# Kernel optimization log

Hardware: AMD Instinct MI355X
Metric: run time of the kernel (lower is better)

Reference implementation:

```python
import jax, jax.numpy as jnp
import numpy as np
import math

D_MODEL = 1024
N_DEVICES = 64
HIDDEN = 128
N_HEADS = 8
B, S = 16, 1024
W_SCALE = 0.02

def setup_inputs() -> dict:
    key = jax.random.key(0)
    ks = jax.random.split(key, 24)
    f = jax.random.normal
    inp = {
        'x': f(ks[0], (B, S, D_MODEL), jnp.float32),
        # attention pooling (n_heads=8, non-causal, self-attention) weights, stored [in,out]
        'wq': f(ks[1], (D_MODEL, D_MODEL), jnp.float32) * W_SCALE,
        'bq': jnp.zeros((D_MODEL,), jnp.float32),
        'wk': f(ks[2], (D_MODEL, D_MODEL), jnp.float32) * W_SCALE,
        'bk': jnp.zeros((D_MODEL,), jnp.float32),
        'wv': f(ks[3], (D_MODEL, D_MODEL), jnp.float32) * W_SCALE,
        'bv': jnp.zeros((D_MODEL,), jnp.float32),
        'wo': f(ks[4], (D_MODEL, D_MODEL), jnp.float32) * W_SCALE,
        'bo': jnp.zeros((D_MODEL,), jnp.float32),
        # device embedding table
        'emb': f(ks[5], (N_DEVICES, D_MODEL), jnp.float32),
        # routing gate: Linear(2d,d) -> Tanh -> Linear(d,N) -> Softmax
        'rg_w1': f(ks[6], (2 * D_MODEL, D_MODEL), jnp.float32) * W_SCALE,
        'rg_b1': jnp.zeros((D_MODEL,), jnp.float32),
        'rg_w2': f(ks[7], (D_MODEL, N_DEVICES), jnp.float32) * W_SCALE,
        'rg_b2': jnp.zeros((N_DEVICES,), jnp.float32),
        'reg_w1': f(ks[8], (N_DEVICES, D_MODEL, HIDDEN), jnp.float32) * W_SCALE,
        'reg_b1': jnp.zeros((N_DEVICES, HIDDEN), jnp.float32),
        'reg_w2': f(ks[9], (N_DEVICES, HIDDEN), jnp.float32) * W_SCALE,
        'reg_b2': jnp.zeros((N_DEVICES,), jnp.float32),
        # stacked per-device classification heads: Linear(d,h)->ReLU->Linear(h,1)->Sigmoid
        'cls_w1': f(ks[10], (N_DEVICES, D_MODEL, HIDDEN), jnp.float32) * W_SCALE,
        'cls_b1': jnp.zeros((N_DEVICES, HIDDEN), jnp.float32),
        'cls_w2': f(ks[11], (N_DEVICES, HIDDEN), jnp.float32) * W_SCALE,
        'cls_b2': jnp.zeros((N_DEVICES,), jnp.float32),
    }
    return inp


def _forward(x, wq, bq, wk, bk, wv, bv, wo, bo, emb,
             rg_w1, rg_b1, rg_w2, rg_b2,
             reg_w1, reg_b1, reg_w2, reg_b2,
             cls_w1, cls_b1, cls_w2, cls_b2):
    b, s, d = x.shape
    dk = d // N_HEADS
    scale = 1.0 / math.sqrt(dk)

    def split_heads(t):  # [b,s,d] -> [b,h,s,dk]
        return t.reshape(b, s, N_HEADS, dk).transpose(0, 2, 1, 3)

    Q = split_heads(x @ wq + bq)
    K = split_heads(x @ wk + bk)
    V = split_heads(x @ wv + bv)
    scores = jnp.einsum('bhqd,bhkd->bhqk', Q, K) * scale
    attn = jax.nn.softmax(scores, axis=-1)  # non-causal, no mask, eval (no dropout)
    ctx = jnp.einsum('bhqk,bhkd->bhqd', attn, V)
    ctx = ctx.transpose(0, 2, 1, 3).reshape(b, s, d)
    pooled = ctx @ wo + bo                       # [b,s,d]
    g = pooled.mean(axis=1)                      # [b,d] global_repr

    g_exp = jnp.broadcast_to(g[:, None, :], (b, N_DEVICES, d))
    de_exp = jnp.broadcast_to(emb[None, :, :], (b, N_DEVICES, d))

    # routing gate
    ri = jnp.concatenate([g_exp, de_exp], axis=-1)        # [b,N,2d]
    h = jnp.tanh(ri @ rg_w1 + rg_b1)                      # [b,N,d]
    rw = jax.nn.softmax(h @ rg_w2 + rg_b2, axis=-1)       # [b,N,N]
    device_repr = jnp.einsum('bnm,md->bnd', rw, emb)      # bmm with expanded embeds
    combined = g_exp + device_repr                        # [b,N,d]

    hr = jax.nn.relu(jnp.einsum('bnd,ndh->bnh', combined, reg_w1) + reg_b1)
    reg = jax.nn.softplus(jnp.einsum('bnh,nh->bn', hr, reg_w2) + reg_b2)

    # per-device classification heads (stacked)
    hc = jax.nn.relu(jnp.einsum('bnd,ndh->bnh', combined, cls_w1) + cls_b1)
    cls = jax.nn.sigmoid(jnp.einsum('bnh,nh->bn', hc, cls_w2) + cls_b2)
    return reg, cls


def reference(x, wq, bq, wk, bk, wv, bv, wo, bo, emb,
              rg_w1, rg_b1, rg_w2, rg_b2,
              reg_w1, reg_b1, reg_w2, reg_b2,
              cls_w1, cls_b1, cls_w2, cls_b2):
    return _forward(x, wq, bq, wk, bk, wv, bv, wo, bo, emb,
                    rg_w1, rg_b1, rg_w2, rg_b2,
                    reg_w1, reg_b1, reg_w2, reg_b2,
                    cls_w1, cls_b1, cls_w2, cls_b2)
```

## Files before the change

### kernel.cpp

```cpp
#include <hip/hip_runtime.h>

typedef unsigned short ushort_t;
typedef __attribute__((ext_vector_type(8))) short short8;
typedef __attribute__((ext_vector_type(4))) float floatx4;

__device__ __forceinline__ ushort_t f2bf(float f) {
    unsigned u = __float_as_uint(f);
    return (ushort_t)((u + 0x7fffu + ((u >> 16) & 1u)) >> 16);
}
__device__ __forceinline__ void gll16(const void* g, void* l) {
    __builtin_amdgcn_global_load_lds(
        (const __attribute__((address_space(1))) unsigned int*)g,
        (__attribute__((address_space(3))) unsigned int*)l, 16, 0, 0);
}

__global__ void prep_kernel(const float* __restrict__ x, ushort_t* __restrict__ xb) {
    size_t i = ((size_t)blockIdx.x * 256 + threadIdx.x) * 8;
    float4 v0 = *(const float4*)(x + i);
    float4 v1 = *(const float4*)(x + i + 4);
    uint4 o;
    o.x = (unsigned)f2bf(v0.x) | ((unsigned)f2bf(v0.y) << 16);
    o.y = (unsigned)f2bf(v0.z) | ((unsigned)f2bf(v0.w) << 16);
    o.z = (unsigned)f2bf(v1.x) | ((unsigned)f2bf(v1.y) << 16);
    o.w = (unsigned)f2bf(v1.z) | ((unsigned)f2bf(v1.w) << 16);
    *(uint4*)(xb + i) = o;
}

__global__ __launch_bounds__(256) void transpose_kernel(
    const float* __restrict__ wq, const float* __restrict__ wk,
    ushort_t* __restrict__ wqT, ushort_t* __restrict__ wkT)
{
    const float* src = blockIdx.z ? wk : wq;
    ushort_t* dst = blockIdx.z ? wkT : wqT;
    const int k0 = blockIdx.x * 64, n0 = blockIdx.y * 64;
    __shared__ float t[64][65];
    const int tid = threadIdx.x;
    const int rr = tid >> 4, cc = (tid & 15) * 4;
#pragma unroll
    for (int p = 0; p < 4; ++p) {
        float4 v = *(const float4*)(src + (size_t)(k0 + p * 16 + rr) * 1024 + n0 + cc);
        t[p * 16 + rr][cc + 0] = v.x;
        t[p * 16 + rr][cc + 1] = v.y;
        t[p * 16 + rr][cc + 2] = v.z;
        t[p * 16 + rr][cc + 3] = v.w;
    }
    __syncthreads();
#pragma unroll
    for (int p = 0; p < 4; ++p) {
        int nl = p * 16 + rr;
        uint2 o;
        o.x = (unsigned)f2bf(t[cc + 0][nl]) | ((unsigned)f2bf(t[cc + 1][nl]) << 16);
        o.y = (unsigned)f2bf(t[cc + 2][nl]) | ((unsigned)f2bf(t[cc + 3][nl]) << 16);
        *(uint2*)(dst + (size_t)(n0 + nl) * 1024 + k0 + cc) = o;
    }
}

__global__ __launch_bounds__(256) void gemm_qk_kernel(
    const ushort_t* __restrict__ xb, const ushort_t* __restrict__ wqT, const ushort_t* __restrict__ wkT,
    const float* __restrict__ bq, const float* __restrict__ bk,
    ushort_t* __restrict__ Qb, ushort_t* __restrict__ Kb)
{
    const int bm = blockIdx.x;
    const int bn = blockIdx.y;
    const int mat = blockIdx.z;
    const ushort_t* W = mat ? wkT : wqT;
    const float* bias = mat ? bk : bq;
    ushort_t* Out = mat ? Kb : Qb;
    const float postscale = mat ? 1.0f : 0.08838834764831845f;

    __shared__ ushort_t a_lds[2][128 * 32];
    __shared__ ushort_t b_lds[2][128 * 32];

    const int tid = threadIdx.x;
    const int lane = tid & 63;
    const int wave = tid >> 6;
    const int wr = wave >> 1, wc = wave & 1;
    const int l16 = lane & 15, quad = lane >> 4;

    floatx4 acc[4][4];
    const floatx4 zero4 = {0.f, 0.f, 0.f, 0.f};
#pragma unroll
    for (int i = 0; i < 4; ++i)
#pragma unroll
        for (int j = 0; j < 4; ++j) acc[i][j] = zero4;

    const int srow = wave * 32 + (lane >> 2);
    const int skof = (lane & 3) * 8;
    const ushort_t* gA = xb + (size_t)(bm * 128 + srow) * 1024 + skof;
    const ushort_t* gB = W + (size_t)(bn * 128 + srow) * 1024 + skof;

    auto issue = [&](int buf, int k0) {
        ushort_t* lA = &a_lds[buf][wave * 1024];
        ushort_t* lB = &b_lds[buf][wave * 1024];
        gll16(gA + k0, lA);
        gll16(gA + k0 + 16 * 1024, lA + 512);
        gll16(gB + k0, lB);
        gll16(gB + k0 + 16 * 1024, lB + 512);
    };

    issue(0, 0);
    for (int kt = 0; kt < 32; ++kt) {
        __syncthreads();
        if (kt < 31) issue((kt + 1) & 1, (kt + 1) * 32);
        const ushort_t* la = a_lds[kt & 1];
        const ushort_t* lb = b_lds[kt & 1];
        short8 afr[4], bfr[4];
#pragma unroll
        for (int mi = 0; mi < 4; ++mi)
            afr[mi] = *(const short8*)&la[(wr * 64 + mi * 16 + l16) * 32 + quad * 8];
#pragma unroll
        for (int ni = 0; ni < 4; ++ni)
            bfr[ni] = *(const short8*)&lb[(wc * 64 + ni * 16 + l16) * 32 + quad * 8];
#pragma unroll
        for (int mi = 0; mi < 4; ++mi)
#pragma unroll
            for (int ni = 0; ni < 4; ++ni)
                acc[mi][ni] = __builtin_amdgcn_mfma_f32_16x16x32_bf16(afr[mi], bfr[ni], acc[mi][ni], 0, 0, 0);
    }
#pragma unroll
    for (int mi = 0; mi < 4; ++mi) {
#pragma unroll
        for (int ni = 0; ni < 4; ++ni) {
            const int gcol = bn * 128 + wc * 64 + ni * 16 + l16;
            const int h = gcol >> 7, d = gcol & 127;
#pragma unroll
            for (int r = 0; r < 4; ++r) {
                const int grow = bm * 128 + wr * 64 + mi * 16 + quad * 4 + r;
                const int b = grow >> 10, s = grow & 1023;
                Out[(((size_t)(b * 8 + h)) * 1024 + s) * 128 + d] =
                    f2bf((acc[mi][ni][r] + bias[gcol]) * postscale);
            }
        }
    }
}

__global__ __launch_bounds__(256, 4) void attn_mfma_kernel(
    const ushort_t* __restrict__ Qb,
    const ushort_t* __restrict__ Kb,
    float* __restrict__ wout)
{
    const int bh = blockIdx.x;
    const int qt = blockIdx.y;
    __shared__ ushort_t ks[2][64 * 128];

    const int tid = threadIdx.x;
    const int wave = tid >> 6, lane = tid & 63;
    const int l16 = lane & 15, quad = lane >> 4;

    const ushort_t* Ksrc = Kb + (size_t)bh * 1024 * 128;

    int srcoff[4];
#pragma unroll
    for (int c = 0; c < 4; ++c) {
        int r = wave * 16 + c * 4 + (lane >> 4);
        int g = (lane & 15) ^ (r & 15);
        srcoff[c] = r * 128 + g * 8;
    }

    auto issue = [&](int buf, int kt) {
        const ushort_t* src = Ksrc + (size_t)kt * 8192;
#pragma unroll
        for (int c = 0; c < 4; ++c)
            gll16(src + srcoff[c], &ks[buf][(wave * 4 + c) * 512]);
    };

    short8 aq[2][4];
    {
        const ushort_t* qsrc = Qb + ((size_t)bh * 1024 + qt * 128 + wave * 32) * 128;
#pragma unroll
        for (int mi = 0; mi < 2; ++mi)
#pragma unroll
            for (int ksp = 0; ksp < 4; ++ksp)
                aq[mi][ksp] = *(const short8*)(qsrc + (size_t)(mi * 16 + l16) * 128 + ksp * 32 + quad * 8);
    }

    const floatx4 zero4 = {0.f, 0.f, 0.f, 0.f};
    float lsum[2][4];
#pragma unroll
    for (int mi = 0; mi < 2; ++mi)
#pragma unroll
        for (int r = 0; r < 4; ++r) lsum[mi][r] = 0.f;

    issue(0, 0);

    for (int kt = 0; kt < 16; ++kt) {
        __syncthreads();
        if (kt < 15) issue((kt + 1) & 1, kt + 1);
        const ushort_t* kbuf = ks[kt & 1];
        floatx4 acc[2][4];
#pragma unroll
        for (int mi = 0; mi < 2; ++mi)
#pragma unroll
            for (int ni = 0; ni < 4; ++ni) acc[mi][ni] = zero4;
#pragma unroll
        for (int ksp = 0; ksp < 4; ++ksp) {
            short8 bk[4];
#pragma unroll
            for (int ni = 0; ni < 4; ++ni) {
                int n = ni * 16 + l16;
                int gs = (ksp * 4 + quad) ^ (n & 15);
                bk[ni] = *(const short8*)&kbuf[n * 128 + gs * 8];
            }
#pragma unroll
            for (int mi = 0; mi < 2; ++mi)
#pragma unroll
                for (int ni = 0; ni < 4; ++ni)
                    acc[mi][ni] = __builtin_amdgcn_mfma_f32_16x16x32_bf16(aq[mi][ksp], bk[ni], acc[mi][ni], 0, 0, 0);
        }
#pragma unroll
        for (int mi = 0; mi < 2; ++mi)
#pragma unroll
            for (int r = 0; r < 4; ++r) {
                float s = 0.f;
#pragma unroll
                for (int ni = 0; ni < 4; ++ni) s += __expf(acc[mi][ni][r]);
                lsum[mi][r] += s;
            }
    }

    issue(0, 0);

    float invl[2][4];
#pragma unroll
    for (int mi = 0; mi < 2; ++mi)
#pragma unroll
        for (int r = 0; r < 4; ++r) {
            float s = lsum[mi][r];
#pragma unroll
            for (int off = 1; off < 16; off <<= 1) s += __shfl_xor(s, off, 16);
            invl[mi][r] = 1.f / s;
        }

    for (int kt = 0; kt < 16; ++kt) {
        __syncthreads();
        if (kt < 15) issue((kt + 1) & 1, kt + 1);
        const ushort_t* kbuf = ks[kt & 1];
        floatx4 acc[2][4];
#pragma unroll
        for (int mi = 0; mi < 2; ++mi)
#pragma unroll
            for (int ni = 0; ni < 4; ++ni) acc[mi][ni] = zero4;
#pragma unroll
        for (int ksp = 0; ksp < 4; ++ksp) {
            short8 bk[4];
#pragma unroll
            for (int ni = 0; ni < 4; ++ni) {
                int n = ni * 16 + l16;
                int gs = (ksp * 4 + quad) ^ (n & 15);
                bk[ni] = *(const short8*)&kbuf[n * 128 + gs * 8];
            }
#pragma unroll
            for (int mi = 0; mi < 2; ++mi)
#pragma unroll
                for (int ni = 0; ni < 4; ++ni)
                    acc[mi][ni] = __builtin_amdgcn_mfma_f32_16x16x32_bf16(aq[mi][ksp], bk[ni], acc[mi][ni], 0, 0, 0);
        }
#pragma unroll
        for (int ni = 0; ni < 4; ++ni) {
            float s = 0.f;
#pragma unroll
            for (int mi = 0; mi < 2; ++mi)
#pragma unroll
                for (int r = 0; r < 4; ++r)
                    s += __expf(acc[mi][ni][r]) * invl[mi][r];
            s += __shfl_xor(s, 16, 64);
            s += __shfl_xor(s, 32, 64);
            if (quad == 0) atomicAdd(&wout[bh * 1024 + kt * 64 + ni * 16 + l16], s);
        }
    }
}

__global__ __launch_bounds__(256) void u_kernel(const ushort_t* __restrict__ xb,
                                                const float* __restrict__ w,
                                                float* __restrict__ u)
{
    const int b = blockIdx.x, kc = blockIdx.y;
    const int c4 = threadIdx.x;
    const ushort_t* Xp = xb + ((size_t)(b * 1024 + kc * 64)) * 1024 + c4 * 4;
    float4 acc[8];
#pragma unroll
    for (int h = 0; h < 8; ++h) acc[h] = make_float4(0.f, 0.f, 0.f, 0.f);
    const float* wb = w + b * 8 * 1024 + kc * 64;
    for (int k = 0; k < 64; ++k) {
        uint2 uv = *(const uint2*)(Xp + (size_t)k * 1024);
        float x0 = __uint_as_float(uv.x << 16);
        float x1 = __uint_as_float(uv.x & 0xffff0000u);
        float x2 = __uint_as_float(uv.y << 16);
        float x3 = __uint_as_float(uv.y & 0xffff0000u);
#pragma unroll
        for (int h = 0; h < 8; ++h) {
            float ww = wb[h * 1024 + k];
            acc[h].x = fmaf(ww, x0, acc[h].x);
            acc[h].y = fmaf(ww, x1, acc[h].y);
            acc[h].z = fmaf(ww, x2, acc[h].z);
            acc[h].w = fmaf(ww, x3, acc[h].w);
        }
    }
#pragma unroll
    for (int h = 0; h < 8; ++h) {
        float* dst = u + ((size_t)(b * 8 + h)) * 1024 + c4 * 4;
        atomicAdd(dst + 0, acc[h].x);
        atomicAdd(dst + 1, acc[h].y);
        atomicAdd(dst + 2, acc[h].z);
        atomicAdd(dst + 3, acc[h].w);
    }
}

__global__ __launch_bounds__(256) void sgemm_kernel(
    const float* __restrict__ A, int lda, long sAz,
    const float* __restrict__ Bm, int ldb, long sBz,
    const float* __restrict__ bias, long sBiasz,
    float* __restrict__ C, int ldc, long sCz,
    int M, int N, int K, float alpha, int nks)
{
    const int z = blockIdx.z;
    const int ks = blockIdx.x % nks;
    const int mt = blockIdx.x / nks;
    const int Kc = K / nks;
    A += (size_t)z * sAz;
    Bm += (size_t)z * sBz;
    C += (size_t)z * sCz;
    const float* bptr = bias ? bias + (size_t)z * sBiasz : nullptr;
    __shared__ float As[64 * 36];
    __shared__ float Bs[32 * 68];
    const int tid = threadIdx.x;
    const int row0 = mt * 64, col0 = blockIdx.y * 64;
    const int ty = tid >> 4, tx = tid & 15;
    float acc[4][4] = {};
    const int aflat = tid * 8;
    const int ar = aflat >> 5, ac = aflat & 31;
    const int br = aflat >> 6, bc = aflat & 63;
    for (int k0 = ks * Kc; k0 < (ks + 1) * Kc; k0 += 32) {
        __syncthreads();
        float4 va0 = make_float4(0.f, 0.f, 0.f, 0.f), va1 = va0;
        if (row0 + ar < M) {
            const float* src = A + (size_t)(row0 + ar) * lda + k0 + ac;
            va0 = *(const float4*)src;
            va1 = *(const float4*)(src + 4);
        }
        *(float4*)&As[ar * 36 + ac] = va0;
        *(float4*)&As[ar * 36 + ac + 4] = va1;
        {
            const float* srcb = Bm + (size_t)(k0 + br) * ldb + col0 + bc;
            *(float4*)&Bs[br * 68 + bc] = *(const float4*)srcb;
            *(float4*)&Bs[br * 68 + bc + 4] = *(const float4*)(srcb + 4);
        }
        __syncthreads();
#pragma unroll
        for (int kk = 0; kk < 32; ++kk) {
            float a0 = As[(ty * 4 + 0) * 36 + kk];
            float a1 = As[(ty * 4 + 1) * 36 + kk];
            float a2 = As[(ty * 4 + 2) * 36 + kk];
            float a3 = As[(ty * 4 + 3) * 36 + kk];
            float b0 = Bs[kk * 68 + tx * 4 + 0];
            float b1 = Bs[kk * 68 + tx * 4 + 1];
            float b2 = Bs[kk * 68 + tx * 4 + 2];
            float b3 = Bs[kk * 68 + tx * 4 + 3];
            acc[0][0] = fmaf(a0, b0, acc[0][0]); acc[0][1] = fmaf(a0, b1, acc[0][1]);
            acc[0][2] = fmaf(a0, b2, acc[0][2]); acc[0][3] = fmaf(a0, b3, acc[0][3]);
            acc[1][0] = fmaf(a1, b0, acc[1][0]); acc[1][1] = fmaf(a1, b1, acc[1][1]);
            acc[1][2] = fmaf(a1, b2, acc[1][2]); acc[1][3] = fmaf(a1, b3, acc[1][3]);
            acc[2][0] = fmaf(a2, b0, acc[2][0]); acc[2][1] = fmaf(a2, b1, acc[2][1]);
            acc[2][2] = fmaf(a2, b2, acc[2][2]); acc[2][3] = fmaf(a2, b3, acc[2][3]);
            acc[3][0] = fmaf(a3, b0, acc[3][0]); acc[3][1] = fmaf(a3, b1, acc[3][1]);
            acc[3][2] = fmaf(a3, b2, acc[3][2]); acc[3][3] = fmaf(a3, b3, acc[3][3]);
        }
    }
#pragma unroll
    for (int i = 0; i < 4; ++i) {
        int r = row0 + ty * 4 + i;
        if (r >= M) continue;
#pragma unroll
        for (int j = 0; j < 4; ++j) {
            int c = col0 + tx * 4 + j;
            float v = alpha * acc[i][j] + ((bptr && ks == 0) ? bptr[c] : 0.f);
            if (nks > 1) atomicAdd(&C[(size_t)r * ldc + c], v);
            else C[(size_t)r * ldc + c] = v;
        }
    }
}

__global__ __launch_bounds__(256) void gate_kernel(
    const float* __restrict__ Ge, const float* __restrict__ Ee, const float* __restrict__ rg_b1,
    const float* __restrict__ rg_w2, const float* __restrict__ rg_b2,
    const float* __restrict__ emb, float* __restrict__ DR)
{
    const int row = blockIdx.x;
    const int b = row >> 6, n = row & 63;
    __shared__ float h[1024];
    __shared__ float red[256];
    __shared__ float rw[64];
    const int tid = threadIdx.x;
    for (int c = tid; c < 1024; c += 256)
        h[c] = tanhf(Ge[b * 1024 + c] + Ee[n * 1024 + c] + rg_b1[c]);
    __syncthreads();
    const int j = tid & 63, ch = tid >> 6;
    float part = 0.f;
    const float* w2p = rg_w2 + (size_t)(ch * 256) * 64 + j;
    for (int c = 0; c < 256; ++c)
        part = fmaf(h[ch * 256 + c], w2p[c * 64], part);
    red[tid] = part;
    __syncthreads();
    if (tid < 64) {
        float lg = red[tid] + red[tid + 64] + red[tid + 128] + red[tid + 192] + rg_b2[j];
        float m = lg;
#pragma unroll
        for (int off = 1; off < 64; off <<= 1) m = fmaxf(m, __shfl_xor(m, off, 64));
        float e = __expf(lg - m);
        float s = e;
#pragma unroll
        for (int off = 1; off < 64; off <<= 1) s += __shfl_xor(s, off, 64);
        rw[tid] = e / s;
    }
    __syncthreads();
    float4 acc = make_float4(0.f, 0.f, 0.f, 0.f);
    const float4* E4 = (const float4*)emb;
    for (int nn = 0; nn < 64; ++nn) {
        float wv = rw[nn];
        float4 ev = E4[nn * 256 + tid];
        acc.x = fmaf(wv, ev.x, acc.x);
        acc.y = fmaf(wv, ev.y, acc.y);
        acc.z = fmaf(wv, ev.z, acc.z);
        acc.w = fmaf(wv, ev.w, acc.w);
    }
    *(float4*)&DR[(size_t)row * 1024 + tid * 4] = acc;
}

__global__ __launch_bounds__(256) void heads_p1_kernel(
    const float* __restrict__ g, const float* __restrict__ DR,
    const float* __restrict__ rw1, const float* __restrict__ cw1,
    float* __restrict__ hpart)
{
    const int n = blockIdx.x, task = blockIdx.y, ksl = blockIdx.z;
    __shared__ float combs[16 * 128];
    const int tid = threadIdx.x;
    for (int i = tid; i < 2048; i += 256) {
        int b = i >> 7, c = i & 127;
        int gc = ksl * 128 + c;
        combs[i] = g[b * 1024 + gc] + DR[((size_t)(b * 64 + n)) * 1024 + gc];
    }
    __syncthreads();
    const int j = tid & 127, sub = tid >> 7;
    const float* W1 = (task ? cw1 : rw1) + (size_t)n * 131072 + (size_t)ksl * 128 * 128;
    float a[8] = {};
    for (int c4 = 0; c4 < 32; ++c4) {
        const float w0 = W1[(c4 * 4 + 0) * 128 + j];
        const float w1 = W1[(c4 * 4 + 1) * 128 + j];
        const float w2 = W1[(c4 * 4 + 2) * 128 + j];
        const float w3 = W1[(c4 * 4 + 3) * 128 + j];
#pragma unroll
        for (int bb = 0; bb < 8; ++bb) {
            float4 cv = *(const float4*)&combs[(sub * 8 + bb) * 128 + c4 * 4];
            a[bb] = fmaf(cv.x, w0, a[bb]);
            a[bb] = fmaf(cv.y, w1, a[bb]);
            a[bb] = fmaf(cv.z, w2, a[bb]);
            a[bb] = fmaf(cv.w, w3, a[bb]);
        }
    }
    float* dst = hpart + (((size_t)(ksl * 2 + task) * 64 + n) * 16 + sub * 8) * 128 + j;
#pragma unroll
    for (int bb = 0; bb < 8; ++bb) dst[bb * 128] = a[bb];
}

__global__ __launch_bounds__(256) void heads_p2_kernel(
    const float* __restrict__ hpart,
    const float* __restrict__ rb1, const float* __restrict__ rw2, const float* __restrict__ rb2,
    const float* __restrict__ cb1, const float* __restrict__ cw2, const float* __restrict__ cb2,
    float* __restrict__ out)
{
    const int n = blockIdx.x, task = blockIdx.y;
    const int tid = threadIdx.x;
    const int b = tid >> 4, jg = tid & 15;
    const float* b1 = (task ? cb1 : rb1) + n * 128 + jg * 8;
    const float* W2 = (task ? cw2 : rw2) + n * 128 + jg * 8;
    float s = 0.f;
#pragma unroll
    for (int k = 0; k < 8; ++k) {
        float h = b1[k];
#pragma unroll
        for (int ksl = 0; ksl < 8; ++ksl)
            h += hpart[(((size_t)(ksl * 2 + task) * 64 + n) * 16 + b) * 128 + jg * 8 + k];
        s = fmaf(fmaxf(h, 0.f), W2[k], s);
    }
#pragma unroll
    for (int off = 1; off < 16; off <<= 1) s += __shfl_xor(s, off, 16);
    if (jg == 0) {
        s += (task ? cb2 : rb2)[n];
        float r = task ? (1.f / (1.f + __expf(-s)))
                       : (fmaxf(s, 0.f) + log1pf(__expf(-fabsf(s))));
        out[task * 1024 + b * 64 + n] = r;
    }
}

extern "C" void kernel_launch(void* const* d_in, const int* in_sizes, int n_in,
                              void* d_out, int out_size, void* d_ws, size_t ws_size,
                              hipStream_t stream)
{
    const float* x      = (const float*)d_in[0];
    const float* wq     = (const float*)d_in[1];
    const float* bq     = (const float*)d_in[2];
    const float* wk     = (const float*)d_in[3];
    const float* bk     = (const float*)d_in[4];
    const float* wv     = (const float*)d_in[5];
    const float* bv     = (const float*)d_in[6];
    const float* wo     = (const float*)d_in[7];
    const float* bo     = (const float*)d_in[8];
    const float* emb    = (const float*)d_in[9];
    const float* rg_w1  = (const float*)d_in[10];
    const float* rg_b1  = (const float*)d_in[11];
    const float* rg_w2  = (const float*)d_in[12];
    const float* rg_b2  = (const float*)d_in[13];
    const float* reg_w1 = (const float*)d_in[14];
    const float* reg_b1 = (const float*)d_in[15];
    const float* reg_w2 = (const float*)d_in[16];
    const float* reg_b2 = (const float*)d_in[17];
    const float* cls_w1 = (const float*)d_in[18];
    const float* cls_b1 = (const float*)d_in[19];
    const float* cls_w2 = (const float*)d_in[20];
    const float* cls_b2 = (const float*)d_in[21];

    char* ws = (char*)d_ws;
    size_t off = 0;
    auto alloc = [&](size_t bytes) { size_t cur = off; off += (bytes + 255) & ~(size_t)255; return cur; };

    ushort_t* xb  = (ushort_t*)(ws + alloc((size_t)16777216 * 2));
    ushort_t* wqT = (ushort_t*)(ws + alloc((size_t)1048576 * 2));
    ushort_t* wkT = (ushort_t*)(ws + alloc((size_t)1048576 * 2));
    ushort_t* Qb  = (ushort_t*)(ws + alloc((size_t)16777216 * 2));
    ushort_t* Kb  = (ushort_t*)(ws + alloc((size_t)16777216 * 2));
    size_t zero_beg = off;
    float* wcol = (float*)(ws + alloc((size_t)131072 * 4));
    float* u    = (float*)(ws + alloc((size_t)131072 * 4));
    float* cm   = (float*)(ws + alloc((size_t)16384 * 4));
    float* gbuf = (float*)(ws + alloc((size_t)16384 * 4));
    float* Ge   = (float*)(ws + alloc((size_t)16384 * 4));
    float* Ee   = (float*)(ws + alloc((size_t)65536 * 4));
    size_t zero_end = off;
    float* DR    = (float*)(ws + alloc((size_t)1048576 * 4));
    float* hpart = (float*)(ws + alloc((size_t)2097152 * 4));

    hipMemsetAsync(ws + zero_beg, 0, zero_end - zero_beg, stream);

    prep_kernel<<<8192, 256, 0, stream>>>(x, xb);
    transpose_kernel<<<dim3(16, 16, 2), 256, 0, stream>>>(wq, wk, wqT, wkT);
    gemm_qk_kernel<<<dim3(128, 8, 2), 256, 0, stream>>>(xb, wqT, wkT, bq, bk, Qb, Kb);
    attn_mfma_kernel<<<dim3(128, 8), 256, 0, stream>>>(Qb, Kb, wcol);
    u_kernel<<<dim3(16, 16), 256, 0, stream>>>(xb, wcol, u);
    sgemm_kernel<<<dim3(4, 2, 8), 256, 0, stream>>>(u, 8192, 1024, wv, 1024, 128, bv, 128,
                                                    cm, 1024, 128, 16, 128, 1024, 1.f / 1024.f, 4);
    sgemm_kernel<<<dim3(8, 16, 1), 256, 0, stream>>>(cm, 1024, 0, wo, 1024, 0, bo, 0,
                                                     gbuf, 1024, 0, 16, 1024, 1024, 1.f, 8);
    sgemm_kernel<<<dim3(8, 16, 1), 256, 0, stream>>>(gbuf, 1024, 0, rg_w1, 1024, 0, nullptr, 0,
                                                     Ge, 1024, 0, 16, 1024, 1024, 1.f, 8);
    sgemm_kernel<<<dim3(8, 16, 1), 256, 0, stream>>>(emb, 1024, 0, rg_w1 + (size_t)1048576, 1024, 0, nullptr, 0,
                                                     Ee, 1024, 0, 64, 1024, 1024, 1.f, 8);
    gate_kernel<<<1024, 256, 0, stream>>>(Ge, Ee, rg_b1, rg_w2, rg_b2, emb, DR);
    heads_p1_kernel<<<dim3(64, 2, 8), 256, 0, stream>>>(gbuf, DR, reg_w1, cls_w1, hpart);
    heads_p2_kernel<<<dim3(64, 2), 256, 0, stream>>>(hpart, reg_b1, reg_w2, reg_b2,
                                                     cls_b1, cls_w2, cls_b2, (float*)d_out);
    (void)in_sizes; (void)n_in; (void)out_size; (void)ws_size;
}
```

Before: 529.7 us.

## Swizzle QK GEMM LDS, fold log2e into Q scale, read K directly in attention

```diff
diff --git a/kernel.cpp b/kernel.cpp
--- a/kernel.cpp
+++ b/kernel.cpp
@@ -13,6 +13,11 @@
         (const __attribute__((address_space(1))) unsigned int*)g,
         (__attribute__((address_space(3))) unsigned int*)l, 16, 0, 0);
 }
+#if __has_builtin(__builtin_amdgcn_exp2f)
+#define EXP2f(x) __builtin_amdgcn_exp2f(x)
+#else
+#define EXP2f(x) exp2f(x)
+#endif
 
 __global__ void prep_kernel(const float* __restrict__ x, ushort_t* __restrict__ xb) {
     size_t i = ((size_t)blockIdx.x * 256 + threadIdx.x) * 8;
@@ -66,7 +71,7 @@
     const ushort_t* W = mat ? wkT : wqT;
     const float* bias = mat ? bk : bq;
     ushort_t* Out = mat ? Kb : Qb;
-    const float postscale = mat ? 1.0f : 0.08838834764831845f;
+    const float postscale = mat ? 1.0f : 0.12751744900508692f;
 
     __shared__ ushort_t a_lds[2][128 * 32];
     __shared__ ushort_t b_lds[2][128 * 32];
@@ -76,6 +81,7 @@
     const int wave = tid >> 6;
     const int wr = wave >> 1, wc = wave & 1;
     const int l16 = lane & 15, quad = lane >> 4;
+    const int qs = quad ^ ((l16 >> 1) & 3);
 
     floatx4 acc[4][4];
     const floatx4 zero4 = {0.f, 0.f, 0.f, 0.f};
@@ -85,7 +91,7 @@
         for (int j = 0; j < 4; ++j) acc[i][j] = zero4;
 
     const int srow = wave * 32 + (lane >> 2);
-    const int skof = (lane & 3) * 8;
+    const int skof = ((lane & 3) ^ ((lane >> 3) & 3)) * 8;
     const ushort_t* gA = xb + (size_t)(bm * 128 + srow) * 1024 + skof;
     const ushort_t* gB = W + (size_t)(bn * 128 + srow) * 1024 + skof;
 
@@ -98,40 +104,49 @@
         gll16(gB + k0 + 16 * 1024, lB + 512);
     };
 
-    issue(0, 0);
-    for (int kt = 0; kt < 32; ++kt) {
-        __syncthreads();
-        if (kt < 31) issue((kt + 1) & 1, (kt + 1) * 32);
-        const ushort_t* la = a_lds[kt & 1];
-        const ushort_t* lb = b_lds[kt & 1];
+    auto compute = [&](int buf) {
+        const ushort_t* la = a_lds[buf];
+        const ushort_t* lb = b_lds[buf];
         short8 afr[4], bfr[4];
 #pragma unroll
         for (int mi = 0; mi < 4; ++mi)
-            afr[mi] = *(const short8*)&la[(wr * 64 + mi * 16 + l16) * 32 + quad * 8];
+            afr[mi] = *(const short8*)&la[(wr * 64 + mi * 16 + l16) * 32 + qs * 8];
 #pragma unroll
         for (int ni = 0; ni < 4; ++ni)
-            bfr[ni] = *(const short8*)&lb[(wc * 64 + ni * 16 + l16) * 32 + quad * 8];
+            bfr[ni] = *(const short8*)&lb[(wc * 64 + ni * 16 + l16) * 32 + qs * 8];
 #pragma unroll
         for (int mi = 0; mi < 4; ++mi)
 #pragma unroll
             for (int ni = 0; ni < 4; ++ni)
                 acc[mi][ni] = __builtin_amdgcn_mfma_f32_16x16x32_bf16(afr[mi], bfr[ni], acc[mi][ni], 0, 0, 0);
-    }
-#pragma unroll
-    for (int mi = 0; mi < 4; ++mi) {
+    };
+
+    issue(0, 0);
+#pragma unroll 4
+    for (int kt = 0; kt < 31; ++kt) {
+        __syncthreads();
+        issue((kt + 1) & 1, (kt + 1) * 32);
+        compute(kt & 1);
+    }
+    __syncthreads();
+    compute(1);
+
+    const int bq_ = bm >> 3;
+    const int sb = (bm & 7) * 128 + wr * 64 + quad * 4;
+    const int dc = wc * 64 + l16;
+    float bp[4];
+#pragma unroll
+    for (int ni = 0; ni < 4; ++ni) bp[ni] = bias[bn * 128 + dc + ni * 16] * postscale;
+    ushort_t* ob = Out + ((size_t)(bq_ * 8 + bn) * 1024 + sb) * 128 + dc;
+#pragma unroll
+    for (int mi = 0; mi < 4; ++mi)
 #pragma unroll
         for (int ni = 0; ni < 4; ++ni) {
-            const int gcol = bn * 128 + wc * 64 + ni * 16 + l16;
-            const int h = gcol >> 7, d = gcol & 127;
-#pragma unroll
-            for (int r = 0; r < 4; ++r) {
-                const int grow = bm * 128 + wr * 64 + mi * 16 + quad * 4 + r;
-                const int b = grow >> 10, s = grow & 1023;
-                Out[(((size_t)(b * 8 + h)) * 1024 + s) * 128 + d] =
-                    f2bf((acc[mi][ni][r] + bias[gcol]) * postscale);
-            }
-        }
-    }
+            ushort_t* p = ob + mi * 2048 + ni * 16;
+#pragma unroll
+            for (int r = 0; r < 4; ++r)
+                p[r * 128] = f2bf(fmaf(acc[mi][ni][r], postscale, bp[ni]));
+        }
 }
 
 __global__ __launch_bounds__(256, 4) void attn_mfma_kernel(
@@ -141,28 +156,11 @@
 {
     const int bh = blockIdx.x;
     const int qt = blockIdx.y;
-    __shared__ ushort_t ks[2][64 * 128];
-
     const int tid = threadIdx.x;
     const int wave = tid >> 6, lane = tid & 63;
     const int l16 = lane & 15, quad = lane >> 4;
 
-    const ushort_t* Ksrc = Kb + (size_t)bh * 1024 * 128;
-
-    int srcoff[4];
-#pragma unroll
-    for (int c = 0; c < 4; ++c) {
-        int r = wave * 16 + c * 4 + (lane >> 4);
-        int g = (lane & 15) ^ (r & 15);
-        srcoff[c] = r * 128 + g * 8;
-    }
-
-    auto issue = [&](int buf, int kt) {
-        const ushort_t* src = Ksrc + (size_t)kt * 8192;
-#pragma unroll
-        for (int c = 0; c < 4; ++c)
-            gll16(src + srcoff[c], &ks[buf][(wave * 4 + c) * 512]);
-    };
+    const ushort_t* Kp = Kb + (size_t)bh * (1024 * 128);
 
     short8 aq[2][4];
     {
@@ -181,12 +179,8 @@
 #pragma unroll
         for (int r = 0; r < 4; ++r) lsum[mi][r] = 0.f;
 
-    issue(0, 0);
-
     for (int kt = 0; kt < 16; ++kt) {
-        __syncthreads();
-        if (kt < 15) issue((kt + 1) & 1, kt + 1);
-        const ushort_t* kbuf = ks[kt & 1];
+        const ushort_t* kb = Kp + (size_t)(kt * 64) * 128;
         floatx4 acc[2][4];
 #pragma unroll
         for (int mi = 0; mi < 2; ++mi)
@@ -194,18 +188,17 @@
             for (int ni = 0; ni < 4; ++ni) acc[mi][ni] = zero4;
 #pragma unroll
         for (int ksp = 0; ksp < 4; ++ksp) {
-            short8 bk[4];
-#pragma unroll
-            for (int ni = 0; ni < 4; ++ni) {
-                int n = ni * 16 + l16;
-                int gs = (ksp * 4 + quad) ^ (n & 15);
-                bk[ni] = *(const short8*)&kbuf[n * 128 + gs * 8];
-            }
+            short8 bkf[4];
+#pragma unroll
+            for (int ni = 0; ni < 4; ++ni)
+                bkf[ni] = *(const short8*)(kb + (size_t)(ni * 16 + l16) * 128 + ksp * 32 + quad * 8);
+            __builtin_amdgcn_s_setprio(1);
 #pragma unroll
             for (int mi = 0; mi < 2; ++mi)
 #pragma unroll
                 for (int ni = 0; ni < 4; ++ni)
-                    acc[mi][ni] = __builtin_amdgcn_mfma_f32_16x16x32_bf16(aq[mi][ksp], bk[ni], acc[mi][ni], 0, 0, 0);
+                    acc[mi][ni] = __builtin_amdgcn_mfma_f32_16x16x32_bf16(aq[mi][ksp], bkf[ni], acc[mi][ni], 0, 0, 0);
+            __builtin_amdgcn_s_setprio(0);
         }
 #pragma unroll
         for (int mi = 0; mi < 2; ++mi)
@@ -213,13 +206,11 @@
             for (int r = 0; r < 4; ++r) {
                 float s = 0.f;
 #pragma unroll
-                for (int ni = 0; ni < 4; ++ni) s += __expf(acc[mi][ni][r]);
+                for (int ni = 0; ni < 4; ++ni) s += EXP2f(acc[mi][ni][r]);
                 lsum[mi][r] += s;
             }
     }
 
-    issue(0, 0);
-
     float invl[2][4];
 #pragma unroll
     for (int mi = 0; mi < 2; ++mi)
@@ -232,9 +223,7 @@
         }
 
     for (int kt = 0; kt < 16; ++kt) {
-        __syncthreads();
-        if (kt < 15) issue((kt + 1) & 1, kt + 1);
-        const ushort_t* kbuf = ks[kt & 1];
+        const ushort_t* kb = Kp + (size_t)(kt * 64) * 128;
         floatx4 acc[2][4];
 #pragma unroll
         for (int mi = 0; mi < 2; ++mi)
@@ -242,18 +231,17 @@
             for (int ni = 0; ni < 4; ++ni) acc[mi][ni] = zero4;
 #pragma unroll
         for (int ksp = 0; ksp < 4; ++ksp) {
-            short8 bk[4];
-#pragma unroll
-            for (int ni = 0; ni < 4; ++ni) {
-                int n = ni * 16 + l16;
-                int gs = (ksp * 4 + quad) ^ (n & 15);
-                bk[ni] = *(const short8*)&kbuf[n * 128 + gs * 8];
-            }
+            short8 bkf[4];
+#pragma unroll
+            for (int ni = 0; ni < 4; ++ni)
+                bkf[ni] = *(const short8*)(kb + (size_t)(ni * 16 + l16) * 128 + ksp * 32 + quad * 8);
+            __builtin_amdgcn_s_setprio(1);
 #pragma unroll
             for (int mi = 0; mi < 2; ++mi)
 #pragma unroll
                 for (int ni = 0; ni < 4; ++ni)
-                    acc[mi][ni] = __builtin_amdgcn_mfma_f32_16x16x32_bf16(aq[mi][ksp], bk[ni], acc[mi][ni], 0, 0, 0);
+                    acc[mi][ni] = __builtin_amdgcn_mfma_f32_16x16x32_bf16(aq[mi][ksp], bkf[ni], acc[mi][ni], 0, 0, 0);
+            __builtin_amdgcn_s_setprio(0);
         }
 #pragma unroll
         for (int ni = 0; ni < 4; ++ni) {
@@ -262,7 +250,7 @@
             for (int mi = 0; mi < 2; ++mi)
 #pragma unroll
                 for (int r = 0; r < 4; ++r)
-                    s += __expf(acc[mi][ni][r]) * invl[mi][r];
+                    s += EXP2f(acc[mi][ni][r]) * invl[mi][r];
             s += __shfl_xor(s, 16, 64);
             s += __shfl_xor(s, 32, 64);
             if (quad == 0) atomicAdd(&wout[bh * 1024 + kt * 64 + ni * 16 + l16], s);
```

Result: slower. 658.7 us (+24.4%).
